# Kernel tuning notes

Hardware: AMD Instinct MI355X
Metric: run time of the kernel (lower is better)

Reference implementation:

```python
import jax, jax.numpy as jnp
import numpy as np
from jax.scipy.special import i0

B, P = 2, 524288
N = (512, 512)            # uniform frequency grid
M = 4                     # window cutoff m (2M taps per dim)
SIGMA = 2.0
NGRID = tuple(2 * (int(SIGMA * Ni) // 2) for Ni in N)  # oversampled grid (1024, 1024)
BETA = tuple(float(np.pi * (2.0 - 1.0 / (ng / Ni))) for ng, Ni in zip(NGRID, N))


def _phi_hat_1d(Ni, ni, b):
    # Fourier coefficients of the Kaiser-Bessel window, k = -Ni/2 .. Ni/2-1
    k = jnp.arange(-Ni // 2, Ni // 2, dtype=jnp.float32)
    arg = jnp.sqrt(b * b - (2.0 * jnp.pi * k / ni) ** 2)
    return i0(M * arg) / ni


def _window_ft():
    # separable d-dim Fourier coefficient grid, shape [N1, N2] (== window.ft)
    c1 = _phi_hat_1d(N[0], NGRID[0], BETA[0])
    c2 = _phi_hat_1d(N[1], NGRID[1], BETA[1])
    return c1[:, None] * c2[None, :]


def _phi(t, ni, b):
    # Kaiser-Bessel window in time domain, support |t| <= M/ni
    u2 = M * M - (ni * t) ** 2
    u = jnp.sqrt(jnp.maximum(u2, 1e-12))
    return jnp.where(u2 > 0, jnp.sinh(b * u) / (jnp.pi * u), 0.0)


def setup_inputs() -> dict:
    key = jax.random.key(0)
    k1, k2 = jax.random.split(key)
    x = jax.random.uniform(k1, (B, P, 2), jnp.float32, -0.5, 0.5)  # points on torus
    f_hat = jax.random.normal(k2, (B, N[0], N[1], 2), jnp.float32)  # complex as [re,im]
    return {"x": x, "f_hat": f_hat}


def _nfft_forward(x, f_hat):
    # f(x_j) ~= sum_k f_hat[k] exp(-2 pi i <k, x_j>) via window-deconvolved oversampled FFT + local gather
    fh = (f_hat[..., 0] + 1j * f_hat[..., 1]).astype(jnp.complex64)  # [B, N1, N2]
    ft = _window_ft().astype(jnp.float32)
    gh = fh / ft                                                    # deconvolve
    p1 = (NGRID[0] - N[0]) // 2
    p2 = (NGRID[1] - N[1]) // 2
    gh = jnp.pad(gh, ((0, 0), (p1, p1), (p2, p2)))                  # centered zero-pad to n
    g = jnp.fft.fftn(jnp.fft.ifftshift(gh, axes=(-2, -1)), axes=(-2, -1))
    g = g / (NGRID[0] * NGRID[1])                                   # g_l = (1/n) sum_k gh_k e^{-2pi i kl/n}

    offs = jnp.arange(-M + 1, M + 1)                                # [2M]
    ws, idxs = [], []
    for d in range(2):
        nd = NGRID[d]
        xd = x[..., d]                                              # [B, P]
        l0 = jnp.floor(xd * nd).astype(jnp.int32)
        l = l0[..., None] + offs                                    # [B, P, 2M]
        t = xd[..., None] - l.astype(jnp.float32) / nd
        ws.append(_phi(t, nd, BETA[d]))
        idxs.append(jnp.mod(l, nd))

    g_flat = g.reshape(B, NGRID[0] * NGRID[1])
    acc = jnp.zeros((B, P), jnp.complex64)
    for i in range(2 * M):                                          # fixed 2m x 2m taps
        for j in range(2 * M):
            flat = idxs[0][..., i] * NGRID[1] + idxs[1][..., j]     # [B, P]
            gv = jnp.take_along_axis(g_flat, flat, axis=1)
            acc = acc + (ws[0][..., i] * ws[1][..., j]) * gv
    return jnp.stack([acc.real, acc.imag], axis=-1)                 # [B, P, 2]


def reference(x, f_hat):
    return _nfft_forward(x, f_hat)
```

## Files before the change

### kernel.cpp

```cpp
#include <hip/hip_runtime.h>

constexpr int   BATCH = 2;
constexpr int   NPTS  = 524288;
constexpr int   BINS  = 2048;
constexpr int   CAP   = 768;
constexpr float BETA  = 4.71238898038469f;
constexpr float PI_F  = 3.14159265358979f;

typedef float v2f __attribute__((ext_vector_type(2)));

#define PIDX(i) ((i) + ((i) >> 4))

constexpr size_t G_BYTES  = (size_t)BATCH * 1024 * 1024 * sizeof(v2f);
constexpr size_t GCNT_OFF = G_BYTES;
constexpr size_t PERM_OFF = G_BYTES + 8192;

__device__ __forceinline__ float i0f_large(float x) {
    float t = 3.75f / x;
    float p =  0.00392377f;
    p = p * t + -0.01647633f;
    p = p * t +  0.02635537f;
    p = p * t + -0.02057706f;
    p = p * t +  0.00916281f;
    p = p * t + -0.00157565f;
    p = p * t +  0.00225319f;
    p = p * t +  0.01328592f;
    p = p * t +  0.39894228f;
    return __expf(x) * rsqrtf(x) * p;
}

__device__ __forceinline__ int tile_of(v2f xv, int b) {
    int c1 = ((int)floorf(xv.x * 1024.0f)) & 1023;
    int c2 = ((int)floorf(xv.y * 1024.0f)) & 1023;
    return (b << 10) + ((c1 >> 5) << 5) + (c2 >> 5);
}

__device__ __forceinline__ v2f cmul4(v2f a, float4 t) {
    v2f lo = {t.x, t.y}, hi = {t.z, t.w};
    return a.x * lo + a.y * hi;
}
__device__ __forceinline__ v2f irot(v2f b) { return (v2f){-b.y, b.x}; }

__device__ __forceinline__ int digitrev4_10(int f) {
    unsigned r = __brev((unsigned)f) >> 22;
    return (int)(((r & 0x2AAu) >> 1) | ((r & 0x155u) << 1));
}

__device__ __forceinline__ void build_tw4(float4* T, int tid, int nthreads) {
    int off = 0, q = 256, sig = 1;
    #pragma unroll
    for (int st = 0; st < 5; ++st) {
        for (int m = tid; m < 3 * q; m += nthreads) {
            int sec = 0, j = m;
            if (j >= q) { sec++; j -= q; }
            if (j >= q) { sec++; j -= q; }
            float ang = (-2.0f * PI_F / 1024.0f) * (float)((sec + 1) * j * sig);
            float sw, cw;
            __sincosf(ang, &sw, &cw);
            T[off + m] = make_float4(cw, sw, -sw, cw);
        }
        off += 3 * q; q >>= 2; sig <<= 2;
    }
}

__device__ __forceinline__ void bfly4(v2f* s, const float4* T,
                                      int bt, int q, int off) {
    int j    = bt & (q - 1);
    int base = ((bt - j) << 2) + j;
    int p0 = PIDX(base), p1 = PIDX(base + q);
    int p2 = PIDX(base + 2 * q), p3 = PIDX(base + 3 * q);
    v2f a0 = s[p0], a1 = s[p1], a2 = s[p2], a3 = s[p3];
    v2f t0 = a0 + a2, t1 = a0 - a2, t2 = a1 + a3, t3 = a1 - a3;
    v2f r3 = irot(t3);
    s[p0] = t0 + t2;
    s[p1] = cmul4(t1 - r3, T[off + j]);
    s[p2] = cmul4(t0 - t2, T[off + q + j]);
    s[p3] = cmul4(t1 + r3, T[off + 2 * q + j]);
}

__global__ __launch_bounds__(256) void rows_and_bin(const v2f* __restrict__ fh,
                                                    v2f* __restrict__ g,
                                                    const v2f* __restrict__ x,
                                                    int* __restrict__ gcnt,
                                                    float4* __restrict__ perm) {
    __shared__ __align__(16) char smem[25072];
    int tid = threadIdx.x;

    if (blockIdx.x < 1024) {
        if (blockIdx.x == 0) {
            #pragma unroll
            for (int i = 0; i < 8; ++i)
                atomicExch(&gcnt[tid * 8 + i], 0);
        }
        v2f*    s = (v2f*)smem;
        float4* T = (float4*)(smem + 8704);
        int blk = blockIdx.x & 511;
        int b   = blockIdx.x >> 9;
        int row = (blk < 256) ? blk : blk + 512;
        int a1  = (row + 256) & 1023;

        build_tw4(T, tid, 256);

        float k1 = (float)(a1 - 256);
        float w1 = (2.0f * PI_F / 1024.0f) * k1;
        float c1 = i0f_large(4.0f * sqrtf(BETA * BETA - w1 * w1));

        const v2f* fr = fh + ((long)b << 18) + ((long)a1 << 9);

        float w2a = (2.0f * PI_F / 1024.0f) * (float)tid;
        float c2a = i0f_large(4.0f * sqrtf(BETA * BETA - w2a * w2a));
        float w2b = (2.0f * PI_F / 1024.0f) * (float)(tid - 256);
        float c2b = i0f_large(4.0f * sqrtf(BETA * BETA - w2b * w2b));

        v2f A = fr[tid + 256] * (1.0f / (c1 * c2a));
        v2f B = fr[tid]       * (1.0f / (c1 * c2b));

        __syncthreads();

        v2f rB = irot(B);
        s[PIDX(tid)]       = A + B;
        s[PIDX(tid + 256)] = cmul4(A + rB, T[tid]);
        s[PIDX(tid + 512)] = cmul4(A - B,  T[256 + tid]);
        s[PIDX(tid + 768)] = cmul4(A - rB, T[512 + tid]);

        int off = 768, q = 64;
        #pragma unroll
        for (int st = 0; st < 4; ++st) {
            __syncthreads();
            bfly4(s, T, tid, q, off);
            off += 3 * q; q >>= 2;
        }
        __syncthreads();

        v2f* base = g + ((long)b << 20) + ((long)row << 10);
        #pragma unroll
        for (int i = 0; i < 4; ++i) {
            int idx = tid + (i << 8);
            base[idx] = s[PIDX(digitrev4_10(idx))];
        }
    } else {
        int* h = (int*)smem;
        int bblk = blockIdx.x - 1024;
        for (int i = tid; i < BINS; i += 256) h[i] = 0;
        __syncthreads();

        int base = bblk * 4096;
        int tile[16];
        v2f pv[16];
        #pragma unroll
        for (int i = 0; i < 16; ++i) {
            int gid = base + tid + i * 256;
            pv[i]   = x[gid];
            tile[i] = tile_of(pv[i], gid >> 19);
            atomicAdd(&h[tile[i]], 1);
        }
        __syncthreads();

        #pragma unroll
        for (int j = 0; j < 8; ++j) {
            int bi = tid + j * 256;
            int c  = h[bi];
            h[bi]  = c ? atomicAdd(&gcnt[bi], c) : 0;
        }
        __syncthreads();

        #pragma unroll
        for (int i = 0; i < 16; ++i) {
            int gid = base + tid + i * 256;
            int pos = atomicAdd(&h[tile[i]], 1);
            perm[tile[i] * CAP + pos] =
                make_float4(pv[i].x, pv[i].y, __int_as_float(gid), 0.0f);
        }
    }
}

__global__ __launch_bounds__(256) void fft_cols(v2f* __restrict__ g) {
    constexpr int STR = 1092;
    __shared__ v2f    s[4 * STR];
    __shared__ float4 T[1023];
    int b  = blockIdx.y;
    int C0 = blockIdx.x * 4;
    int t  = threadIdx.x;
    int c  = t & 3, L = t >> 2;
    v2f* gb = g + ((long)b << 20);

    build_tw4(T, t, 256);

    v2f E[16];
    #pragma unroll
    for (int m = 0; m < 4; ++m) {
        int r = L + 64 * m;
        E[m] = gb[((long)r << 10) + C0 + c];
    }
    #pragma unroll
    for (int m = 12; m < 16; ++m) {
        int r = L + 64 * m;
        E[m] = gb[((long)r << 10) + C0 + c];
    }
    __syncthreads();

    #pragma unroll
    for (int m = 0; m < 4; ++m) {
        v2f A = E[m], B = E[m + 12];
        v2f rB = irot(B);
        int j = L + 64 * m;
        E[m]      = A + B;
        E[m + 4]  = cmul4(A + rB, T[j]);
        E[m + 8]  = cmul4(A - B,  T[256 + j]);
        E[m + 12] = cmul4(A - rB, T[512 + j]);
    }

    {
        float4 u1 = T[768 + L], u2 = T[768 + 64 + L], u3 = T[768 + 128 + L];
        #pragma unroll
        for (int a = 0; a < 4; ++a) {
            v2f a0 = E[4*a], a1 = E[4*a+1], a2 = E[4*a+2], a3 = E[4*a+3];
            v2f t0 = a0 + a2, t1 = a0 - a2, t2 = a1 + a3, t3 = a1 - a3;
            v2f r3 = irot(t3);
            E[4*a]   = t0 + t2;
            E[4*a+1] = cmul4(t1 - r3, u1);
            E[4*a+2] = cmul4(t0 - t2, u2);
            E[4*a+3] = cmul4(t1 + r3, u3);
        }
    }

    v2f* sf = s + c * STR;
    #pragma unroll
    for (int m = 0; m < 16; ++m) sf[PIDX(L + 64 * m)] = E[m];
    __syncthreads();

    #pragma unroll
    for (int rr = 0; rr < 4; ++rr)
        bfly4(sf, T, L + rr * 64, 16, 960);
    __syncthreads();

    v2f C[16];
    int cb = 17 * L;
    #pragma unroll
    for (int j = 0; j < 16; ++j) C[j] = sf[cb + j];

    #pragma unroll
    for (int j = 0; j < 4; ++j) {
        v2f a0 = C[j], a1 = C[j+4], a2 = C[j+8], a3 = C[j+12];
        v2f t0 = a0 + a2, t1 = a0 - a2, t2 = a1 + a3, t3 = a1 - a3;
        v2f r3 = irot(t3);
        C[j]    = t0 + t2;
        C[j+4]  = cmul4(t1 - r3, T[1008 + j]);
        C[j+8]  = cmul4(t0 - t2, T[1012 + j]);
        C[j+12] = cmul4(t1 + r3, T[1016 + j]);
    }
    #pragma unroll
    for (int e = 0; e < 4; ++e) {
        v2f a0 = C[4*e], a1 = C[4*e+1], a2 = C[4*e+2], a3 = C[4*e+3];
        v2f t0 = a0 + a2, t1 = a0 - a2, t2 = a1 + a3, t3 = a1 - a3;
        v2f r3 = irot(t3);
        C[4*e]   = t0 + t2;
        C[4*e+1] = t1 - r3;
        C[4*e+2] = t0 - t2;
        C[4*e+3] = t1 + r3;
    }

    #pragma unroll
    for (int j = 0; j < 16; ++j) {
        int r = digitrev4_10((L << 4) + j);
        gb[((long)r << 10) + C0 + c] = C[j];
    }
}

__global__ __launch_bounds__(256) void gather_binned(const v2f* __restrict__ g,
                                                     const int* __restrict__ gcnt,
                                                     const float4* __restrict__ perm,
                                                     v2f* __restrict__ out) {
    __shared__ v2f patch[37 * 37];
    int tb = blockIdx.x;
    int b  = tb >> 10;
    int tt = tb & 1023;
    int tR = tt >> 5, tC = tt & 31;
    int R0 = (tR << 5) - 2, C0 = (tC << 5) - 2;
    const v2f* gb = g + ((long)b << 20);

    for (int p = threadIdx.x; p < 37 * 37; p += 256) {
        int pr = p / 37, pc = p - pr * 37;
        int gr = (R0 + pr) & 1023, gc = (C0 + pc) & 1023;
        patch[p] = gb[(gr << 10) + gc];
    }
    __syncthreads();

    int cnt = gcnt[tb];
    if (cnt > CAP) cnt = CAP;
    int off0 = tb * CAP;
    for (int i = (int)threadIdx.x; i < cnt; i += 256) {
        float4 rec = perm[off0 + i];
        int gid = __float_as_int(rec.z);

        float w1[6], w2[6];
        int rr0, cc0;
        {
            float xs = rec.x * 1024.0f;
            float fl = floorf(xs);
            float fr = xs - fl;
            rr0 = (((int)fl) & 1023) - (tR << 5);
            #pragma unroll
            for (int k = 0; k < 6; ++k) {
                float tv = fr - (float)(k - 2);
                float u2 = 16.0f - tv * tv;
                float ir = rsqrtf(u2);
                float z  = BETA * u2 * ir;
                w1[k] = __expf(z) * 0.159154943f * ir;
            }
        }
        {
            float xs = rec.y * 1024.0f;
            float fl = floorf(xs);
            float fr = xs - fl;
            cc0 = (((int)fl) & 1023) - (tC << 5);
            #pragma unroll
            for (int k = 0; k < 6; ++k) {
                float tv = fr - (float)(k - 2);
                float u2 = 16.0f - tv * tv;
                float ir = rsqrtf(u2);
                float z  = BETA * u2 * ir;
                w2[k] = __expf(z) * 0.159154943f * ir;
            }
        }

        v2f acc = {0.0f, 0.0f};
        #pragma unroll
        for (int ii = 0; ii < 6; ++ii) {
            int pbase = (rr0 + ii) * 37 + cc0;
            float wi = w1[ii];
            #pragma unroll
            for (int jj = 0; jj < 6; ++jj)
                acc += (wi * w2[jj]) * patch[pbase + jj];
        }
        out[gid] = acc;
    }
}

extern "C" void kernel_launch(void* const* d_in, const int* in_sizes, int n_in,
                              void* d_out, int out_size, void* d_ws, size_t ws_size,
                              hipStream_t stream) {
    const v2f* x  = (const v2f*)d_in[0];
    const v2f* fh = (const v2f*)d_in[1];
    char* ws = (char*)d_ws;
    v2f*    g    = (v2f*)ws;
    int*    gcnt = (int*)(ws + GCNT_OFF);
    float4* perm = (float4*)(ws + PERM_OFF);

    rows_and_bin<<<dim3(1280), dim3(256), 0, stream>>>(fh, g, x, gcnt, perm);
    fft_cols    <<<dim3(256, BATCH), dim3(256), 0, stream>>>(g);

    gather_binned<<<dim3(BINS), dim3(256), 0, stream>>>(g, gcnt, perm, (v2f*)d_out);
}
```

Baseline: 115.5 us.

## Compute first-stage FFT twiddles in registers, shrink twiddle tables and LDS

The row and column FFT kernels no longer build a full 1023-entry twiddle table in shared memory. First-stage twiddles are now computed per thread with sincos plus complex multiplies, and only the small later-stage tables are kept. This cuts LDS use in rows_and_bin from about 25KB to about 12.8KB, which should allow more resident blocks, and it removes most of the twiddle-building work. The binning branch now gives each block half as many points, with 512 binning blocks instead of 256, to spread that work wider. The cost is more register arithmetic and slightly different twiddle rounding.

```diff
diff --git a/kernel.cpp b/kernel.cpp
--- a/kernel.cpp
+++ b/kernel.cpp
@@ -40,20 +40,24 @@
     return a.x * lo + a.y * hi;
 }
 __device__ __forceinline__ v2f irot(v2f b) { return (v2f){-b.y, b.x}; }
+__device__ __forceinline__ v2f cmulv(v2f a, v2f b) {
+    return (v2f){a.x * b.x - a.y * b.y, a.x * b.y + a.y * b.x};
+}
+__device__ __forceinline__ float4 tw4p(v2f w) {
+    return make_float4(w.x, w.y, -w.y, w.x);
+}
 
 __device__ __forceinline__ int digitrev4_10(int f) {
     unsigned r = __brev((unsigned)f) >> 22;
     return (int)(((r & 0x2AAu) >> 1) | ((r & 0x155u) << 1));
 }
 
-__device__ __forceinline__ void build_tw4(float4* T, int tid, int nthreads) {
-    int off = 0, q = 256, sig = 1;
-    #pragma unroll
-    for (int st = 0; st < 5; ++st) {
+__device__ __forceinline__ void build_tw_small(float4* T, int tid, int nthreads,
+                                               int q0, int sig0, int nst) {
+    int off = 0, q = q0, sig = sig0;
+    for (int st = 0; st < nst; ++st) {
         for (int m = tid; m < 3 * q; m += nthreads) {
-            int sec = 0, j = m;
-            if (j >= q) { sec++; j -= q; }
-            if (j >= q) { sec++; j -= q; }
+            int sec = m / q, j = m - sec * q;
             float ang = (-2.0f * PI_F / 1024.0f) * (float)((sec + 1) * j * sig);
             float sw, cw;
             __sincosf(ang, &sw, &cw);
@@ -83,7 +87,7 @@
                                                     const v2f* __restrict__ x,
                                                     int* __restrict__ gcnt,
                                                     float4* __restrict__ perm) {
-    __shared__ __align__(16) char smem[25072];
+    __shared__ __align__(16) char smem[12784];
     int tid = threadIdx.x;
 
     if (blockIdx.x < 1024) {
@@ -99,7 +103,7 @@
         int row = (blk < 256) ? blk : blk + 512;
         int a1  = (row + 256) & 1023;
 
-        build_tw4(T, tid, 256);
+        build_tw_small(T, tid, 256, 64, 4, 4);
 
         float k1 = (float)(a1 - 256);
         float w1 = (2.0f * PI_F / 1024.0f) * k1;
@@ -115,15 +119,21 @@
         v2f A = fr[tid + 256] * (1.0f / (c1 * c2a));
         v2f B = fr[tid]       * (1.0f / (c1 * c2b));
 
+        float sw0, cw0;
+        __sincosf((-2.0f * PI_F / 1024.0f) * (float)tid, &sw0, &cw0);
+        v2f wt = {cw0, sw0};
+        v2f wt2 = cmulv(wt, wt);
+        v2f wt3 = cmulv(wt2, wt);
+
         __syncthreads();
 
         v2f rB = irot(B);
         s[PIDX(tid)]       = A + B;
-        s[PIDX(tid + 256)] = cmul4(A + rB, T[tid]);
-        s[PIDX(tid + 512)] = cmul4(A - B,  T[256 + tid]);
-        s[PIDX(tid + 768)] = cmul4(A - rB, T[512 + tid]);
-
-        int off = 768, q = 64;
+        s[PIDX(tid + 256)] = cmul4(A + rB, tw4p(wt));
+        s[PIDX(tid + 512)] = cmul4(A - B,  tw4p(wt2));
+        s[PIDX(tid + 768)] = cmul4(A - rB, tw4p(wt3));
+
+        int off = 0, q = 64;
         #pragma unroll
         for (int st = 0; st < 4; ++st) {
             __syncthreads();
@@ -144,11 +154,11 @@
         for (int i = tid; i < BINS; i += 256) h[i] = 0;
         __syncthreads();
 
-        int base = bblk * 4096;
-        int tile[16];
-        v2f pv[16];
-        #pragma unroll
-        for (int i = 0; i < 16; ++i) {
+        int base = bblk * 2048;
+        int tile[8];
+        v2f pv[8];
+        #pragma unroll
+        for (int i = 0; i < 8; ++i) {
             int gid = base + tid + i * 256;
             pv[i]   = x[gid];
             tile[i] = tile_of(pv[i], gid >> 19);
@@ -165,7 +175,7 @@
         __syncthreads();
 
         #pragma unroll
-        for (int i = 0; i < 16; ++i) {
+        for (int i = 0; i < 8; ++i) {
             int gid = base + tid + i * 256;
             int pos = atomicAdd(&h[tile[i]], 1);
             perm[tile[i] * CAP + pos] =
@@ -177,14 +187,14 @@
 __global__ __launch_bounds__(256) void fft_cols(v2f* __restrict__ g) {
     constexpr int STR = 1092;
     __shared__ v2f    s[4 * STR];
-    __shared__ float4 T[1023];
+    __shared__ float4 Tsm[60];
     int b  = blockIdx.y;
     int C0 = blockIdx.x * 4;
     int t  = threadIdx.x;
     int c  = t & 3, L = t >> 2;
     v2f* gb = g + ((long)b << 20);
 
-    build_tw4(T, t, 256);
+    build_tw_small(Tsm, t, 256, 16, 16, 2);
 
     v2f E[16];
     #pragma unroll
@@ -197,21 +207,32 @@
         int r = L + 64 * m;
         E[m] = gb[((long)r << 10) + C0 + c];
     }
-    __syncthreads();
+
+    float sL, cL;
+    __sincosf((-2.0f * PI_F / 1024.0f) * (float)L, &sL, &cL);
+    v2f wL = {cL, sL};
+    const v2f R1 = {0.923879533f, -0.382683432f};
+    const v2f R2 = {0.707106781f, -0.707106781f};
+    const v2f R3 = {0.382683432f, -0.923879533f};
 
     #pragma unroll
     for (int m = 0; m < 4; ++m) {
+        v2f w1 = (m == 0) ? wL : cmulv(wL, (m == 1) ? R1 : (m == 2) ? R2 : R3);
+        v2f w2 = cmulv(w1, w1);
+        v2f w3 = cmulv(w2, w1);
         v2f A = E[m], B = E[m + 12];
         v2f rB = irot(B);
-        int j = L + 64 * m;
         E[m]      = A + B;
-        E[m + 4]  = cmul4(A + rB, T[j]);
-        E[m + 8]  = cmul4(A - B,  T[256 + j]);
-        E[m + 12] = cmul4(A - rB, T[512 + j]);
+        E[m + 4]  = cmul4(A + rB, tw4p(w1));
+        E[m + 8]  = cmul4(A - B,  tw4p(w2));
+        E[m + 12] = cmul4(A - rB, tw4p(w3));
     }
 
     {
-        float4 u1 = T[768 + L], u2 = T[768 + 64 + L], u3 = T[768 + 128 + L];
+        v2f p  = cmulv(wL, wL); p = cmulv(p, p);
+        v2f p2 = cmulv(p, p);
+        v2f p3 = cmulv(p2, p);
+        float4 u1 = tw4p(p), u2 = tw4p(p2), u3 = tw4p(p3);
         #pragma unroll
         for (int a = 0; a < 4; ++a) {
             v2f a0 = E[4*a], a1 = E[4*a+1], a2 = E[4*a+2], a3 = E[4*a+3];
@@ -224,6 +245,7 @@
         }
     }
 
+    __syncthreads();
     v2f* sf = s + c * STR;
     #pragma unroll
     for (int m = 0; m < 16; ++m) sf[PIDX(L + 64 * m)] = E[m];
@@ -231,7 +253,7 @@
 
     #pragma unroll
     for (int rr = 0; rr < 4; ++rr)
-        bfly4(sf, T, L + rr * 64, 16, 960);
+        bfly4(sf, Tsm, L + rr * 64, 16, 0);
     __syncthreads();
 
     v2f C[16];
@@ -245,9 +267,9 @@
         v2f t0 = a0 + a2, t1 = a0 - a2, t2 = a1 + a3, t3 = a1 - a3;
         v2f r3 = irot(t3);
         C[j]    = t0 + t2;
-        C[j+4]  = cmul4(t1 - r3, T[1008 + j]);
-        C[j+8]  = cmul4(t0 - t2, T[1012 + j]);
-        C[j+12] = cmul4(t1 + r3, T[1016 + j]);
+        C[j+4]  = cmul4(t1 - r3, Tsm[48 + j]);
+        C[j+8]  = cmul4(t0 - t2, Tsm[52 + j]);
+        C[j+12] = cmul4(t1 + r3, Tsm[56 + j]);
     }
     #pragma unroll
     for (int e = 0; e < 4; ++e) {
@@ -347,7 +369,7 @@
     int*    gcnt = (int*)(ws + GCNT_OFF);
     float4* perm = (float4*)(ws + PERM_OFF);
 
-    rows_and_bin<<<dim3(1280), dim3(256), 0, stream>>>(fh, g, x, gcnt, perm);
+    rows_and_bin<<<dim3(1536), dim3(256), 0, stream>>>(fh, g, x, gcnt, perm);
     fft_cols    <<<dim3(256, BATCH), dim3(256), 0, stream>>>(g);
 
     gather_binned<<<dim3(BINS), dim3(256), 0, stream>>>(g, gcnt, perm, (v2f*)d_out);
```

Measured after the change: 117.2 us. Within noise of the previous version (+1.5%).
